# Optimization experiments

Measured on AMD Instinct MI355X. Metric: run time of the kernel, lower is better.

Reference implementation:

```python
import jax, jax.numpy as jnp
import numpy as np

D_MODEL = 128; N_HEADS = 8; N_LEVELS = 1; N_POINTS = 8
MAX_RES = 10.0
B, H_SP, W_SP = 8, 64, 64


def setup_inputs() -> dict:
    key = jax.random.key(0)
    ks = jax.random.split(key, 8)
    s = 0.02
    f32 = jnp.float32
    return {
        "nbr_fea": jax.random.normal(ks[0], (B, D_MODEL, H_SP, W_SP), f32),
        "ext_fea": jax.random.normal(ks[1], (B, D_MODEL, H_SP, W_SP), f32),
        "W_val": jax.random.normal(ks[2], (D_MODEL, D_MODEL), f32) * s,
        "b_val": jnp.zeros((D_MODEL,), f32),
        "W_off": jax.random.normal(ks[3], (D_MODEL, N_HEADS * N_LEVELS * N_POINTS * 2), f32) * s,
        "b_off": jax.random.normal(ks[4], (N_HEADS * N_LEVELS * N_POINTS * 2,), f32) * s,
        "W_attn": jax.random.normal(ks[5], (D_MODEL, N_HEADS * N_LEVELS * N_POINTS), f32) * s,
        "b_attn": jnp.zeros((N_HEADS * N_LEVELS * N_POINTS,), f32),
        "W_out": jax.random.normal(ks[6], (D_MODEL, D_MODEL), f32) * s,
        "b_out": jnp.zeros((D_MODEL,), f32),
    }


def _deform_attn_align(nbr_fea, ext_fea, W_val, b_val, W_off, b_off, W_attn, b_attn, W_out, b_out):
    b, c, h, w = nbr_fea.shape
    L = h * w
    dh = c // N_HEADS
    # flatten b c h w -> b (h w) c
    query = jnp.transpose(ext_fea, (0, 2, 3, 1)).reshape(b, L, c)
    vin = jnp.transpose(nbr_fea, (0, 2, 3, 1)).reshape(b, L, c)

    # value projection (mask is all-False -> no masked fill needed)
    value = (vin @ W_val + b_val).reshape(b, L, N_HEADS, dh)
    vh = jnp.transpose(value, (0, 2, 1, 3))  # [b, H, L, dh]

    # sampling offsets, clamped by max_residue_magnitude * tanh
    off = MAX_RES * jnp.tanh(query @ W_off + b_off)
    off = off.reshape(b, L, N_HEADS, N_POINTS, 2)  # single level
    attn = jax.nn.softmax((query @ W_attn + b_attn).reshape(b, L, N_HEADS, N_POINTS), axis=-1)

    # reference points in [0,1]; valid_ratio == 1 since padding mask is all-False
    yy, xx = jnp.meshgrid(jnp.arange(h, dtype=jnp.float32), jnp.arange(w, dtype=jnp.float32), indexing="ij")
    ref = jnp.stack([(xx.reshape(-1) + 0.5) / w, (yy.reshape(-1) + 0.5) / h], axis=-1)  # [L, 2]
    norm = jnp.array([w, h], jnp.float32)  # offset_normalizer [W, H]
    loc = ref[None, :, None, None, :] + off / norm  # [b, L, H, P, 2]

    # grid_sample(align_corners=False, padding_mode='zeros') pixel coordinates
    px = jnp.transpose(loc[..., 0] * w - 0.5, (0, 2, 1, 3))  # [b, H, L, P]
    py = jnp.transpose(loc[..., 1] * h - 0.5, (0, 2, 1, 3))

    x0 = jnp.floor(px); y0 = jnp.floor(py)
    fx = px - x0; fy = py - y0
    x0i = x0.astype(jnp.int32); y0i = y0.astype(jnp.int32)

    def gather(xi, yi):
        valid = (xi >= 0) & (xi < w) & (yi >= 0) & (yi < h)
        idx = jnp.clip(yi, 0, h - 1) * w + jnp.clip(xi, 0, w - 1)  # [b, H, L, P]
        g = jnp.take_along_axis(vh, idx.reshape(b, N_HEADS, L * N_POINTS)[..., None], axis=2)
        return g.reshape(b, N_HEADS, L, N_POINTS, dh) * valid[..., None]

    samp = (gather(x0i, y0i) * ((1.0 - fx) * (1.0 - fy))[..., None]
            + gather(x0i + 1, y0i) * (fx * (1.0 - fy))[..., None]
            + gather(x0i, y0i + 1) * ((1.0 - fx) * fy)[..., None]
            + gather(x0i + 1, y0i + 1) * (fx * fy)[..., None])  # [b, H, L, P, dh]

    aw = jnp.transpose(attn, (0, 2, 1, 3))  # [b, H, L, P]
    out = jnp.sum(samp * aw[..., None], axis=3)  # [b, H, L, dh]
    out = jnp.transpose(out, (0, 2, 1, 3)).reshape(b, L, c)
    out = out @ W_out + b_out
    return jnp.transpose(out.reshape(b, h, w, c), (0, 3, 1, 2))  # b c h w


def reference(nbr_fea, ext_fea, W_val, b_val, W_off, b_off, W_attn, b_attn, W_out, b_out):
    return _deform_attn_align(nbr_fea, ext_fea, W_val, b_val, W_off, b_off, W_attn, b_attn, W_out, b_out)
```

## Files before the change

kernel.cpp:

```cpp
#include <hip/hip_runtime.h>
#include <cstdint>

#define HB 8
#define CM 128
#define NHEAD 8
#define NPT 8
#define DHD 16
#define HS 64
#define WS 64
#define LTOT 4096
#define NQA 192
#define QAP 192
#define LFP 132

typedef float floatx4 __attribute__((ext_vector_type(4)));
typedef short bf16x8 __attribute__((ext_vector_type(8)));

__device__ __forceinline__ unsigned short f2bf_rne(float x) {
  unsigned u = __float_as_uint(x);
  return (unsigned short)((u + 0x7FFFu + ((u >> 16) & 1)) >> 16);
}
__device__ __forceinline__ void split_bf(float x, unsigned short& h, unsigned short& l) {
  unsigned u = __float_as_uint(x);
  h = (unsigned short)(u >> 16);
  float r = x - __uint_as_float(u & 0xFFFF0000u);
  l = (unsigned short)(__float_as_uint(r) >> 16);
}
__device__ __forceinline__ float fast_tanh(float x) {
  float e = __expf(2.0f * x);
  return 1.0f - 2.0f / (e + 1.0f);
}

__global__ __launch_bounds__(256) void prep(const float* __restrict__ Wv,
                                            const float* __restrict__ Wo,
                                            const float* __restrict__ Wa,
                                            const float* __restrict__ Ww,
                                            const float* __restrict__ bo,
                                            const float* __restrict__ ba,
                                            unsigned short* __restrict__ wf_val,
                                            unsigned short* __restrict__ wf_qa,
                                            unsigned short* __restrict__ wf_out,
                                            float* __restrict__ bias_qa) {
  const int gid = blockIdx.x * 256 + threadIdx.x;
  const int k4 = gid / 448;
  const int ng = gid - k4 * 448;

  const float* src;
  unsigned short* dst;
  int Nsrc, Nn, nd, n;
  if (ng < 128) {        src = Wv; dst = wf_val; Nsrc = 128; Nn = 128; n = ng;        nd = n; }
  else if (ng < 256) {   src = Wo; dst = wf_qa;  Nsrc = 128; Nn = 192; n = ng - 128;  nd = n; }
  else if (ng < 320) {   src = Wa; dst = wf_qa;  Nsrc = 64;  Nn = 192; n = ng - 256;  nd = n + 128; }
  else {                 src = Ww; dst = wf_out; Nsrc = 128; Nn = 128; n = ng - 320;  nd = n; }

  ushort4 hi, lo;
  split_bf(src[(k4 * 4 + 0) * Nsrc + n], hi.x, lo.x);
  split_bf(src[(k4 * 4 + 1) * Nsrc + n], hi.y, lo.y);
  split_bf(src[(k4 * 4 + 2) * Nsrc + n], hi.z, lo.z);
  split_bf(src[(k4 * 4 + 3) * Nsrc + n], hi.w, lo.w);
  const int off = (k4 >> 1) * Nn * 8 + nd * 8 + (k4 & 1) * 4;
  *(ushort4*)(dst + off) = hi;
  *(ushort4*)(dst + Nn * 128 + off) = lo;

  if (gid < 128) bias_qa[gid] = bo[gid];
  else if (gid < 192) bias_qa[gid] = ba[gid - 128];
}

__global__ __launch_bounds__(256, 4) void gemm_val(const float* __restrict__ nbr,
                                                   const unsigned short* __restrict__ WF,
                                                   const float* __restrict__ bias,
                                                   unsigned short* __restrict__ value) {
  __shared__ char smem[33792];
  unsigned short* AB = (unsigned short*)smem;
  const int t = threadIdx.x;
  const int ml0 = blockIdx.x * 64;
  const int b = blockIdx.y;

  {
    const float* src = nbr + (size_t)b * CM * LTOT + ml0;
    const int x = t & 63, kq = t >> 6;
#pragma unroll
    for (int i = 0; i < 8; i++) {
      const int kb = kq * 4 + i * 16;
      ushort4 hi, lo;
      split_bf(src[(size_t)(kb + 0) * LTOT + x], hi.x, lo.x);
      split_bf(src[(size_t)(kb + 1) * LTOT + x], hi.y, lo.y);
      split_bf(src[(size_t)(kb + 2) * LTOT + x], hi.z, lo.z);
      split_bf(src[(size_t)(kb + 3) * LTOT + x], hi.w, lo.w);
      const int off = x * 128 + (((kb >> 3) ^ (x & 15)) << 3) + (kb & 7);
      *(ushort4*)(AB + off) = hi;
      *(ushort4*)(AB + 8192 + off) = lo;
    }
  }
  __syncthreads();

  const int w = t >> 6, lane = t & 63;
  const int wm = (w >> 1) * 32, wn = (w & 1) * 64;
  const int nl = lane & 15, q = lane >> 4;

  floatx4 acc[2][4];
#pragma unroll
  for (int mt = 0; mt < 2; mt++)
#pragma unroll
    for (int j = 0; j < 4; j++) acc[mt][j] = {0.0f, 0.0f, 0.0f, 0.0f};

#pragma unroll
  for (int K0 = 0; K0 < 4; K0++) {
    bf16x8 ah[2], al[2];
#pragma unroll
    for (int mt = 0; mt < 2; mt++) {
      const int m = wm + mt * 16 + nl;
      const int off = m * 128 + (((K0 * 4 + q) ^ (m & 15)) << 3);
      ah[mt] = *(bf16x8*)(AB + off);
      al[mt] = *(bf16x8*)(AB + 8192 + off);
    }
#pragma unroll
    for (int j = 0; j < 4; j++) {
      const size_t o = (size_t)(K0 * 4 + q) * CM * 8 + (wn + j * 16 + nl) * 8;
      const bf16x8 wh = *(const bf16x8*)(WF + o);
      const bf16x8 wl = *(const bf16x8*)(WF + (size_t)CM * 128 + o);
#pragma unroll
      for (int mt = 0; mt < 2; mt++) {
        acc[mt][j] = __builtin_amdgcn_mfma_f32_16x16x32_bf16(al[mt], wh, acc[mt][j], 0, 0, 0);
        acc[mt][j] = __builtin_amdgcn_mfma_f32_16x16x32_bf16(ah[mt], wl, acc[mt][j], 0, 0, 0);
        acc[mt][j] = __builtin_amdgcn_mfma_f32_16x16x32_bf16(ah[mt], wh, acc[mt][j], 0, 0, 0);
      }
    }
  }

  __syncthreads();
  float* LF = (float*)smem;
#pragma unroll
  for (int j = 0; j < 4; j++) {
    const int gc = wn + j * 16 + nl;
    const float bv = bias[gc];
#pragma unroll
    for (int mt = 0; mt < 2; mt++)
#pragma unroll
      for (int r = 0; r < 4; r++)
        LF[(wm + mt * 16 + q * 4 + r) * LFP + gc] = acc[mt][j][r] + bv;
  }
  __syncthreads();
#pragma unroll
  for (int i = 0; i < 4; i++) {
    const int c = t + i * 256;
    const int h = c >> 7, rem = c & 127, l = rem >> 1, half = rem & 1;
    const float* sp = LF + l * LFP + h * 16 + half * 8;
    uint4 st;
    st.x = ((unsigned)f2bf_rne(sp[1]) << 16) | f2bf_rne(sp[0]);
    st.y = ((unsigned)f2bf_rne(sp[3]) << 16) | f2bf_rne(sp[2]);
    st.z = ((unsigned)f2bf_rne(sp[5]) << 16) | f2bf_rne(sp[4]);
    st.w = ((unsigned)f2bf_rne(sp[7]) << 16) | f2bf_rne(sp[6]);
    *(uint4*)(value + ((size_t)(b * NHEAD + h) * LTOT + ml0 + l) * DHD + half * 8) = st;
  }
}

__global__ __launch_bounds__(256, 4) void samp(const float* __restrict__ ext,
                                               const unsigned short* __restrict__ value,
                                               const unsigned short* __restrict__ wf_qa,
                                               const unsigned short* __restrict__ wf_out,
                                               const float* __restrict__ bias_qa,
                                               const float* __restrict__ b_out,
                                               float* __restrict__ out) {
  __shared__ char smem[40960];
  unsigned short* AB = (unsigned short*)smem;
  float* qaT = (float*)(smem + 16384);
  float2* WXY = (float2*)smem;
  float* WA = (float*)(smem + 16384);
  unsigned short* FR = (unsigned short*)(smem + 24576);

  const int t = threadIdx.x;
  const int b = blockIdx.x & 7;
  const int ml0 = (blockIdx.x >> 3) * 32;
  const int w = t >> 6, lane = t & 63;
  const int nl = lane & 15, q = lane >> 4;

  {
    const float* src = ext + (size_t)b * CM * LTOT + ml0;
    const int x = t & 31, kq = t >> 5;
#pragma unroll
    for (int i = 0; i < 4; i++) {
      const int kb = i * 32 + kq * 4;
      ushort4 hi, lo;
      split_bf(src[(size_t)(kb + 0) * LTOT + x], hi.x, lo.x);
      split_bf(src[(size_t)(kb + 1) * LTOT + x], hi.y, lo.y);
      split_bf(src[(size_t)(kb + 2) * LTOT + x], hi.z, lo.z);
      split_bf(src[(size_t)(kb + 3) * LTOT + x], hi.w, lo.w);
      const int off = x * 128 + (((kb >> 3) ^ (x & 15)) << 3) + (kb & 7);
      *(ushort4*)(AB + off) = hi;
      *(ushort4*)(AB + 4096 + off) = lo;
    }
  }
  __syncthreads();

  {
    const int wm = (w & 1) * 16;
    const int wn = (w >> 1) * 96;
    floatx4 acc[6];
#pragma unroll
    for (int j = 0; j < 6; j++) acc[j] = {0.0f, 0.0f, 0.0f, 0.0f};
#pragma unroll
    for (int K0 = 0; K0 < 4; K0++) {
      const int m = wm + nl;
      const int off = m * 128 + (((K0 * 4 + q) ^ (m & 15)) << 3);
      const bf16x8 ah = *(bf16x8*)(AB + off);
      const bf16x8 al = *(bf16x8*)(AB + 4096 + off);
#pragma unroll
      for (int j = 0; j < 6; j++) {
        const size_t o = (size_t)(K0 * 4 + q) * NQA * 8 + (wn + j * 16 + nl) * 8;
        const bf16x8 wh = *(const bf16x8*)(wf_qa + o);
        const bf16x8 wl = *(const bf16x8*)(wf_qa + (size_t)NQA * 128 + o);
        acc[j] = __builtin_amdgcn_mfma_f32_16x16x32_bf16(al, wh, acc[j], 0, 0, 0);
        acc[j] = __builtin_amdgcn_mfma_f32_16x16x32_bf16(ah, wl, acc[j], 0, 0, 0);
        acc[j] = __builtin_amdgcn_mfma_f32_16x16x32_bf16(ah, wh, acc[j], 0, 0, 0);
      }
    }
#pragma unroll
    for (int j = 0; j < 6; j++) {
      const int n = wn + j * 16 + nl;
      const float bv = bias_qa[n];
#pragma unroll
      for (int r = 0; r < 4; r++)
        qaT[(wm + q * 4 + r) * QAP + n] = acc[j][r] + bv;
    }
  }
  __syncthreads();

  {
    const int ll = t >> 3, h = t & 7;
    const float* qrow = qaT + ll * QAP;
    float4 of[4];
#pragma unroll
    for (int j = 0; j < 4; j++) of[j] = *(const float4*)(qrow + h * 16 + j * 4);
    const float4 lga = *(const float4*)(qrow + 128 + h * 8);
    const float4 lgb = *(const float4*)(qrow + 128 + h * 8 + 4);
    __syncthreads();
    const float lg[8] = {lga.x, lga.y, lga.z, lga.w, lgb.x, lgb.y, lgb.z, lgb.w};
    float m = lg[0];
#pragma unroll
    for (int p = 1; p < 8; p++) m = fmaxf(m, lg[p]);
    float e[8], s = 0.0f;
#pragma unroll
    for (int p = 0; p < 8; p++) { e[p] = __expf(lg[p] - m); s += e[p]; }
    const float inv = 1.0f / s;
    const int l = ml0 + ll;
    const float xf = (float)(l & (WS - 1));
    const float yf = (float)(l >> 6);
#pragma unroll
    for (int p = 0; p < 8; p++) {
      const float ox = (p & 1) ? of[p >> 1].z : of[p >> 1].x;
      const float oy = (p & 1) ? of[p >> 1].w : of[p >> 1].y;
      WXY[p * 256 + t] = {xf + 10.0f * fast_tanh(ox), yf + 10.0f * fast_tanh(oy)};
      WA[p * 256 + t] = e[p] * inv;
    }
  }
  __syncthreads();

  {
    const int d4 = t & 3;
    const int u = t >> 2;
#pragma unroll
    for (int ps = 0; ps < 4; ps++) {
      const int uu = ps * 64 + u;
      const int ll = uu >> 3;
      const int h = uu & 7;
      const unsigned short* vbb = value + ((size_t)(b * NHEAD + h) * LTOT) * DHD + d4 * 4;

      float4 o = {0.0f, 0.0f, 0.0f, 0.0f};
#pragma unroll
      for (int p = 0; p < 8; p++) {
        const float2 pxy = WXY[p * 256 + uu];
        const float aw = WA[p * 256 + uu];
        const float x0f = floorf(pxy.x), y0f = floorf(pxy.y);
        const float fx = pxy.x - x0f, fy = pxy.y - y0f;
        const int ix = (int)x0f, iy = (int)y0f;
#pragma unroll
        for (int c = 0; c < 4; c++) {
          const int cdx = c & 1, cdy = c >> 1;
          const int jx = ix + cdx, jy = iy + cdy;
          const float wx = cdx ? fx : 1.0f - fx;
          const float wy = cdy ? fy : 1.0f - fy;
          const bool valid = ((unsigned)jx < WS) & ((unsigned)jy < HS);
          const float wc = valid ? aw * wx * wy : 0.0f;
          const int cx = min(max(jx, 0), WS - 1);
          const int cy = min(max(jy, 0), HS - 1);
          const uint2 rw = *(const uint2*)(vbb + (size_t)((cy << 6) + cx) * DHD);
          o.x += wc * __uint_as_float(rw.x << 16);
          o.y += wc * __uint_as_float(rw.x & 0xFFFF0000u);
          o.z += wc * __uint_as_float(rw.y << 16);
          o.w += wc * __uint_as_float(rw.y & 0xFFFF0000u);
        }
      }
      const int off = ll * 128 + (((h * 2 + (d4 >> 1)) ^ (ll & 15)) << 3) + (d4 & 1) * 4;
      ushort4 st = {f2bf_rne(o.x), f2bf_rne(o.y), f2bf_rne(o.z), f2bf_rne(o.w)};
      *(ushort4*)(FR + off) = st;
    }
  }
  __syncthreads();

  {
    const int wm = (w & 1) * 16;
    const int wn = (w >> 1) * 64;
    floatx4 acc[4];
#pragma unroll
    for (int j = 0; j < 4; j++) acc[j] = {0.0f, 0.0f, 0.0f, 0.0f};
#pragma unroll
    for (int K0 = 0; K0 < 4; K0++) {
      const int m = wm + nl;
      const int off = m * 128 + (((K0 * 4 + q) ^ (m & 15)) << 3);
      const bf16x8 ah = *(bf16x8*)(FR + off);
#pragma unroll
      for (int j = 0; j < 4; j++) {
        const int n = wn + j * 16 + nl;
        const size_t o = (size_t)(K0 * 4 + q) * CM * 8 + n * 8;
        const bf16x8 wh = *(const bf16x8*)(wf_out + o);
        const bf16x8 wl = *(const bf16x8*)(wf_out + (size_t)CM * 128 + o);
        acc[j] = __builtin_amdgcn_mfma_f32_16x16x32_bf16(ah, wl, acc[j], 0, 0, 0);
        acc[j] = __builtin_amdgcn_mfma_f32_16x16x32_bf16(ah, wh, acc[j], 0, 0, 0);
      }
    }
#pragma unroll
    for (int j = 0; j < 4; j++) {
      const int gc = wn + j * 16 + nl;
      const float bv = b_out[gc];
      float4 st = {acc[j][0] + bv, acc[j][1] + bv, acc[j][2] + bv, acc[j][3] + bv};
      *(float4*)(out + ((size_t)b * CM + gc) * LTOT + ml0 + wm + q * 4) = st;
    }
  }
}

extern "C" void kernel_launch(void* const* d_in, const int* in_sizes, int n_in,
                              void* d_out, int out_size, void* d_ws, size_t ws_size,
                              hipStream_t stream) {
  const float* nbr    = (const float*)d_in[0];
  const float* ext    = (const float*)d_in[1];
  const float* W_val  = (const float*)d_in[2];
  const float* b_val  = (const float*)d_in[3];
  const float* W_off  = (const float*)d_in[4];
  const float* b_off  = (const float*)d_in[5];
  const float* W_attn = (const float*)d_in[6];
  const float* b_attn = (const float*)d_in[7];
  const float* W_out  = (const float*)d_in[8];
  const float* b_out  = (const float*)d_in[9];
  float* out = (float*)d_out;

  unsigned short* value = (unsigned short*)d_ws;
  unsigned short* wf_val = value + (size_t)HB * NHEAD * LTOT * DHD;
  unsigned short* wf_qa  = wf_val + 128 * 128 * 2;
  unsigned short* wf_out = wf_qa + 192 * 128 * 2;
  float* bias_qa = (float*)(wf_out + 128 * 128 * 2);

  prep<<<56, 256, 0, stream>>>(W_val, W_off, W_attn, W_out, b_off, b_attn,
                               wf_val, wf_qa, wf_out, bias_qa);
  gemm_val<<<dim3(64, HB), 256, 0, stream>>>(nbr, wf_val, b_val, value);
  samp<<<dim3(128 * HB), 256, 0, stream>>>(ext, value, wf_qa, wf_out, bias_qa, b_out, out);
}
```

Baseline: 135.6 us.

## Precompute bilinear corner weights and indices once; gather 16-byte rows per thread

The sampling setup now computes the four masked corner weights and packed clamped corner indices once per (query, head, point) and stores them in shared memory. This replaces having each of four threads recompute floor, validity and clamping. The gather loop now gives each thread 8 channels with 16-byte loads instead of 4 channels with 8-byte loads, halving the number of gather instructions. The shared-memory layout is reorganised, with a larger footprint, padded qa stride and an extra barrier, and the occupancy hint drops from 4 to 3 blocks per CU. This trades some occupancy for less redundant math and wider memory accesses.

```diff
diff --git a/kernel.cpp b/kernel.cpp
--- a/kernel.cpp
+++ b/kernel.cpp
@@ -10,7 +10,7 @@
 #define WS 64
 #define LTOT 4096
 #define NQA 192
-#define QAP 192
+#define QAP 196
 #define LFP 132
 
 typedef float floatx4 __attribute__((ext_vector_type(4)));
@@ -19,6 +19,9 @@
 __device__ __forceinline__ unsigned short f2bf_rne(float x) {
   unsigned u = __float_as_uint(x);
   return (unsigned short)((u + 0x7FFFu + ((u >> 16) & 1)) >> 16);
+}
+__device__ __forceinline__ unsigned pack_bf2(float a, float b) {
+  return ((unsigned)f2bf_rne(b) << 16) | f2bf_rne(a);
 }
 __device__ __forceinline__ void split_bf(float x, unsigned short& h, unsigned short& l) {
   unsigned u = __float_as_uint(x);
@@ -147,27 +150,27 @@
     const int h = c >> 7, rem = c & 127, l = rem >> 1, half = rem & 1;
     const float* sp = LF + l * LFP + h * 16 + half * 8;
     uint4 st;
-    st.x = ((unsigned)f2bf_rne(sp[1]) << 16) | f2bf_rne(sp[0]);
-    st.y = ((unsigned)f2bf_rne(sp[3]) << 16) | f2bf_rne(sp[2]);
-    st.z = ((unsigned)f2bf_rne(sp[5]) << 16) | f2bf_rne(sp[4]);
-    st.w = ((unsigned)f2bf_rne(sp[7]) << 16) | f2bf_rne(sp[6]);
+    st.x = pack_bf2(sp[0], sp[1]);
+    st.y = pack_bf2(sp[2], sp[3]);
+    st.z = pack_bf2(sp[4], sp[5]);
+    st.w = pack_bf2(sp[6], sp[7]);
     *(uint4*)(value + ((size_t)(b * NHEAD + h) * LTOT + ml0 + l) * DHD + half * 8) = st;
   }
 }
 
-__global__ __launch_bounds__(256, 4) void samp(const float* __restrict__ ext,
+__global__ __launch_bounds__(256, 3) void samp(const float* __restrict__ ext,
                                                const unsigned short* __restrict__ value,
                                                const unsigned short* __restrict__ wf_qa,
                                                const unsigned short* __restrict__ wf_out,
                                                const float* __restrict__ bias_qa,
                                                const float* __restrict__ b_out,
                                                float* __restrict__ out) {
-  __shared__ char smem[40960];
+  __shared__ char smem[49152];
   unsigned short* AB = (unsigned short*)smem;
-  float* qaT = (float*)(smem + 16384);
-  float2* WXY = (float2*)smem;
-  float* WA = (float*)(smem + 16384);
-  unsigned short* FR = (unsigned short*)(smem + 24576);
+  float* qaT = (float*)(smem + 8192);
+  float4* W4 = (float4*)smem;
+  unsigned* BAD = (unsigned*)(smem + 32768);
+  unsigned short* FR = (unsigned short*)(smem + 40960);
 
   const int t = threadIdx.x;
   const int b = blockIdx.x & 7;
@@ -215,6 +218,7 @@
         acc[j] = __builtin_amdgcn_mfma_f32_16x16x32_bf16(ah, wh, acc[j], 0, 0, 0);
       }
     }
+    __syncthreads();
 #pragma unroll
     for (int j = 0; j < 6; j++) {
       const int n = wn + j * 16 + nl;
@@ -250,50 +254,69 @@
     for (int p = 0; p < 8; p++) {
       const float ox = (p & 1) ? of[p >> 1].z : of[p >> 1].x;
       const float oy = (p & 1) ? of[p >> 1].w : of[p >> 1].y;
-      WXY[p * 256 + t] = {xf + 10.0f * fast_tanh(ox), yf + 10.0f * fast_tanh(oy)};
-      WA[p * 256 + t] = e[p] * inv;
-    }
-  }
-  __syncthreads();
-
-  {
-    const int d4 = t & 3;
-    const int u = t >> 2;
-#pragma unroll
-    for (int ps = 0; ps < 4; ps++) {
-      const int uu = ps * 64 + u;
+      const float aw = e[p] * inv;
+      const float px = xf + 10.0f * fast_tanh(ox);
+      const float py = yf + 10.0f * fast_tanh(oy);
+      const float x0f = floorf(px), y0f = floorf(py);
+      const float fx = px - x0f, fy = py - y0f;
+      const int ix = (int)x0f, iy = (int)y0f;
+      const float sx0 = ((unsigned)ix < WS) ? (1.0f - fx) : 0.0f;
+      const float sx1 = ((unsigned)(ix + 1) < WS) ? fx : 0.0f;
+      const float sy0 = ((unsigned)iy < HS) ? (1.0f - fy) : 0.0f;
+      const float sy1 = ((unsigned)(iy + 1) < HS) ? fy : 0.0f;
+      const int x0c = min(max(ix, 0), WS - 1);
+      const int y0c = min(max(iy, 0), HS - 1);
+      const int dx = min(max(ix + 1, 0), WS - 1) - x0c;
+      const int dy = min(max(iy + 1, 0), HS - 1) - y0c;
+      const int idx = p * 256 + t;
+      W4[idx] = {aw * sx0 * sy0, aw * sx1 * sy0, aw * sx0 * sy1, aw * sx1 * sy1};
+      BAD[idx] = (unsigned)((y0c << 6) + x0c) | ((unsigned)dx << 12) | ((unsigned)dy << 13);
+    }
+  }
+  __syncthreads();
+
+  {
+    const int d2 = t & 1;
+    const int u = t >> 1;
+#pragma unroll
+    for (int ps = 0; ps < 2; ps++) {
+      const int uu = ps * 128 + u;
       const int ll = uu >> 3;
       const int h = uu & 7;
-      const unsigned short* vbb = value + ((size_t)(b * NHEAD + h) * LTOT) * DHD + d4 * 4;
-
-      float4 o = {0.0f, 0.0f, 0.0f, 0.0f};
+      const unsigned short* vbb = value + ((size_t)(b * NHEAD + h) * LTOT) * DHD + d2 * 8;
+
+      float o[8];
+#pragma unroll
+      for (int j = 0; j < 8; j++) o[j] = 0.0f;
+
 #pragma unroll
       for (int p = 0; p < 8; p++) {
-        const float2 pxy = WXY[p * 256 + uu];
-        const float aw = WA[p * 256 + uu];
-        const float x0f = floorf(pxy.x), y0f = floorf(pxy.y);
-        const float fx = pxy.x - x0f, fy = pxy.y - y0f;
-        const int ix = (int)x0f, iy = (int)y0f;
-#pragma unroll
-        for (int c = 0; c < 4; c++) {
-          const int cdx = c & 1, cdy = c >> 1;
-          const int jx = ix + cdx, jy = iy + cdy;
-          const float wx = cdx ? fx : 1.0f - fx;
-          const float wy = cdy ? fy : 1.0f - fy;
-          const bool valid = ((unsigned)jx < WS) & ((unsigned)jy < HS);
-          const float wc = valid ? aw * wx * wy : 0.0f;
-          const int cx = min(max(jx, 0), WS - 1);
-          const int cy = min(max(jy, 0), HS - 1);
-          const uint2 rw = *(const uint2*)(vbb + (size_t)((cy << 6) + cx) * DHD);
-          o.x += wc * __uint_as_float(rw.x << 16);
-          o.y += wc * __uint_as_float(rw.x & 0xFFFF0000u);
-          o.z += wc * __uint_as_float(rw.y << 16);
-          o.w += wc * __uint_as_float(rw.y & 0xFFFF0000u);
+        const int idx = p * 256 + uu;
+        const float4 wv = W4[idx];
+        const unsigned ub = BAD[idx];
+        const int base = ub & 0xFFF;
+        const int ddx = (ub >> 12) & 1;
+        const int o2b = base + (((ub >> 13) & 1) << 6);
+        const uint4 r0 = *(const uint4*)(vbb + (size_t)base * DHD);
+        const uint4 r1 = *(const uint4*)(vbb + (size_t)(base + ddx) * DHD);
+        const uint4 r2 = *(const uint4*)(vbb + (size_t)o2b * DHD);
+        const uint4 r3 = *(const uint4*)(vbb + (size_t)(o2b + ddx) * DHD);
+#pragma unroll
+        for (int j = 0; j < 4; j++) {
+          const unsigned c0 = (&r0.x)[j], c1 = (&r1.x)[j], c2 = (&r2.x)[j], c3 = (&r3.x)[j];
+          o[j * 2 + 0] += wv.x * __uint_as_float(c0 << 16) + wv.y * __uint_as_float(c1 << 16) +
+                          wv.z * __uint_as_float(c2 << 16) + wv.w * __uint_as_float(c3 << 16);
+          o[j * 2 + 1] += wv.x * __uint_as_float(c0 & 0xFFFF0000u) + wv.y * __uint_as_float(c1 & 0xFFFF0000u) +
+                          wv.z * __uint_as_float(c2 & 0xFFFF0000u) + wv.w * __uint_as_float(c3 & 0xFFFF0000u);
         }
       }
-      const int off = ll * 128 + (((h * 2 + (d4 >> 1)) ^ (ll & 15)) << 3) + (d4 & 1) * 4;
-      ushort4 st = {f2bf_rne(o.x), f2bf_rne(o.y), f2bf_rne(o.z), f2bf_rne(o.w)};
-      *(ushort4*)(FR + off) = st;
+      const int off = ll * 128 + (((h * 2 + d2) ^ (ll & 15)) << 3);
+      uint4 st;
+      st.x = pack_bf2(o[0], o[1]);
+      st.y = pack_bf2(o[2], o[3]);
+      st.z = pack_bf2(o[4], o[5]);
+      st.w = pack_bf2(o[6], o[7]);
+      *(uint4*)(FR + off) = st;
     }
   }
   __syncthreads();
```

New measurement: 172.0 us. 1.27x slower.
